# Performance work log

Hardware: AMD Instinct MI355X
Metric: run time of the kernel (lower is better)

Reference implementation:

```python
import jax, jax.numpy as jnp
import numpy as np

D = 1024        # d_hidden
DE = 512        # d_expert (routed)
E = 8           # n_routed_experts
TOP_K = 2
DS = DE * 2     # shared expert width = d_expert * n_shared_experts


def setup_inputs() -> dict:
    key = jax.random.key(0)
    ks = jax.random.split(key, 8)
    s = 1.0 / np.sqrt(D)
    return {
        "x": jax.random.normal(ks[0], (2, 1024, D), dtype=jnp.float32),
        "W_g": jax.random.normal(ks[1], (D, E), dtype=jnp.float32) * s,
        "Wg_e": jax.random.normal(ks[2], (E, D, DE), dtype=jnp.float32) * s,
        "Wu_e": jax.random.normal(ks[3], (E, D, DE), dtype=jnp.float32) * s,
        "Wd_e": jax.random.normal(ks[4], (E, DE, D), dtype=jnp.float32) * (1.0 / np.sqrt(DE)),
        "Wg_s": jax.random.normal(ks[5], (D, DS), dtype=jnp.float32) * s,
        "Wu_s": jax.random.normal(ks[6], (D, DS), dtype=jnp.float32) * s,
        "Wd_s": jax.random.normal(ks[7], (DS, D), dtype=jnp.float32) * (1.0 / np.sqrt(DS)),
    }


def _moe(x, W_g, Wg_e, Wu_e, Wd_e, Wg_s, Wu_s, Wd_s):
    B, T, Dm = x.shape
    N = B * T
    xf = x.reshape(N, Dm)

    # shared expert (SwiGLU)
    shared = (jax.nn.silu(xf @ Wg_s) * (xf @ Wu_s)) @ Wd_s  # [N, D]

    # gating: softmax then top-k (set membership identical to torch sorted=False)
    probs = jax.nn.softmax(xf @ W_g, axis=-1)               # [N, E]
    topk_vals, topk_ids = jax.lax.top_k(probs, TOP_K)       # [N, K]

    # combine weights c[n, e] = sum of topk_vals where routed to expert e
    # (equivalent to the original gather -> weighted scatter_add combine)
    c = jnp.zeros((N, E), dtype=x.dtype)
    c = c.at[jnp.arange(N)[:, None], topk_ids].add(topk_vals)

    # dense per-expert SwiGLU, weighted-combined (same math as gather/scatter loop)
    gate = jax.nn.silu(jnp.einsum('nd,edh->neh', xf, Wg_e))
    up = jnp.einsum('nd,edh->neh', xf, Wu_e)
    routed = jnp.einsum('neh,ne,ehd->nd', gate * up, c, Wd_e)  # [N, D]

    return (shared + routed).reshape(B, T, Dm)


def reference(x, W_g, Wg_e, Wu_e, Wd_e, Wg_s, Wu_s, Wd_s):
    return _moe(x, W_g, Wg_e, Wu_e, Wd_e, Wg_s, Wu_s, Wd_s)
```

## Files before the change

kernel.cpp:

```cpp
#include <hip/hip_runtime.h>
#include <hip/hip_bf16.h>

#define NTOK 2048
#define DIM  1024
#define DEXP 512
#define NEXP 8
#define DSH  1024
#define KH   5120
#define MAXROWS 5120
#define PACKBLOCKS 3840

typedef __hip_bfloat16 bf16;
typedef __attribute__((ext_vector_type(8))) short bf16x8;
typedef __attribute__((ext_vector_type(4))) float floatx4;

__device__ __forceinline__ void gl_lds16(const bf16* g, bf16* l) {
    __builtin_amdgcn_global_load_lds(
        (const __attribute__((address_space(1))) void*)g,
        (__attribute__((address_space(3))) void*)l, 16, 0, 0);
}

__device__ __forceinline__ float b2f(short s) {
    union { float f; unsigned u; } v;
    v.u = ((unsigned)(unsigned short)s) << 16;
    return v.f;
}

struct B4 { bf16 a, b, c, d; };

__global__ __launch_bounds__(128) void pack_gate(
        const float* __restrict__ Wg_s, const float* __restrict__ Wu_s,
        const float* __restrict__ Wg_e, const float* __restrict__ Wu_e,
        const float* __restrict__ Wd_s, const float* __restrict__ Wd_e,
        const float* __restrict__ x, const float* __restrict__ Wg,
        bf16* __restrict__ Bg, bf16* __restrict__ Bu, bf16* __restrict__ Bd,
        bf16* __restrict__ Xb, int2* __restrict__ te, float2* __restrict__ tp) {
    int b = blockIdx.x;
    const int tid = threadIdx.x;
    if (b < PACKBLOCKS) {
        __shared__ unsigned lt[64][35];
        const float* src; bf16* dst; int C; long dstStride, dstBase; int tilesX;
        if (b < 256)        { src = Wg_s; dst = Bg; C = 1024; dstStride = 1024; dstBase = 0; tilesX = 16; }
        else if (b < 1280)  { int z = (b - 256) >> 7; b = (b - 256) & 127;
                              src = Wg_e + (long)z * DIM * DEXP; dst = Bg; C = 512;
                              dstStride = 1024; dstBase = (long)(DSH + z * DEXP) * 1024; tilesX = 8; }
        else if (b < 1536)  { b -= 1280; src = Wu_s; dst = Bu; C = 1024; dstStride = 1024; dstBase = 0; tilesX = 16; }
        else if (b < 2560)  { int z = (b - 1536) >> 7; b = (b - 1536) & 127;
                              src = Wu_e + (long)z * DIM * DEXP; dst = Bu; C = 512;
                              dstStride = 1024; dstBase = (long)(DSH + z * DEXP) * 1024; tilesX = 8; }
        else if (b < 2816)  { b -= 2560; src = Wd_s; dst = Bd; C = 1024; dstStride = KH; dstBase = 0; tilesX = 16; }
        else                { int z = (b - 2816) >> 7; b = (b - 2816) & 127;
                              src = Wd_e + (long)z * DEXP * DIM; dst = Bd; C = 1024;
                              dstStride = KH; dstBase = DSH + (long)z * DEXP; tilesX = 16; }
        const int tileX = b & (tilesX - 1), tileY = b / tilesX;
        const int c0 = tileX * 64, r0 = tileY * 64;

        const int lrow = tid >> 4, lch = tid & 15;
#pragma unroll
        for (int i = 0; i < 8; i++) {
            int row = lrow + i * 8;
            float4 v = *(const float4*)(src + (long)(r0 + row) * C + c0 + lch * 4);
            union { bf16 h[2]; unsigned u; } p0, p1;
            p0.h[0] = __float2bfloat16(v.x); p0.h[1] = __float2bfloat16(v.y);
            p1.h[0] = __float2bfloat16(v.z); p1.h[1] = __float2bfloat16(v.w);
            lt[row][lch * 2]     = p0.u;
            lt[row][lch * 2 + 1] = p1.u;
        }
        __syncthreads();
        const int kc = tid & 7;
#pragma unroll
        for (int i = 0; i < 4; i++) {
            int h = (tid >> 3) + i * 16;
            union { unsigned short s[8]; bf16x8 v8; } o;
#pragma unroll
            for (int j = 0; j < 8; j++)
                o.s[j] = ((const unsigned short*)lt[kc * 8 + j])[h];
            *(bf16x8*)(dst + dstBase + (long)(c0 + h) * dstStride + r0 + kc * 8) = o.v8;
        }
    } else {
        int t = (b - PACKBLOCKS) * 2 + (tid >> 6);
        int lane = tid & 63;
        const float* xr = x + (long)t * DIM;
        bf16* xo = Xb + (long)t * DIM;
        float acc[NEXP] = {0.f, 0.f, 0.f, 0.f, 0.f, 0.f, 0.f, 0.f};
#pragma unroll
        for (int i = 0; i < 4; i++) {
            int d = lane * 4 + i * 256;
            float4 xv = *(const float4*)(xr + d);
            B4 o{__float2bfloat16(xv.x), __float2bfloat16(xv.y),
                 __float2bfloat16(xv.z), __float2bfloat16(xv.w)};
            *(B4*)(xo + d) = o;
#pragma unroll
            for (int j = 0; j < 4; j++) {
                float xs = (j == 0) ? xv.x : (j == 1) ? xv.y : (j == 2) ? xv.z : xv.w;
                float4 w0 = *(const float4*)(Wg + (d + j) * NEXP);
                float4 w1 = *(const float4*)(Wg + (d + j) * NEXP + 4);
                acc[0] += xs * w0.x; acc[1] += xs * w0.y; acc[2] += xs * w0.z; acc[3] += xs * w0.w;
                acc[4] += xs * w1.x; acc[5] += xs * w1.y; acc[6] += xs * w1.z; acc[7] += xs * w1.w;
            }
        }
#pragma unroll
        for (int e = 0; e < NEXP; e++)
#pragma unroll
            for (int off = 32; off; off >>= 1)
                acc[e] += __shfl_xor(acc[e], off);
        if (lane == 0) {
            float m = acc[0];
#pragma unroll
            for (int e = 1; e < NEXP; e++) m = fmaxf(m, acc[e]);
            float p[NEXP], s = 0.f;
#pragma unroll
            for (int e = 0; e < NEXP; e++) { p[e] = expf(acc[e] - m); s += p[e]; }
            float inv = 1.f / s;
#pragma unroll
            for (int e = 0; e < NEXP; e++) p[e] *= inv;
            int i1 = 0;
#pragma unroll
            for (int e = 1; e < NEXP; e++) if (p[e] > p[i1]) i1 = e;
            int i2 = (i1 == 0) ? 1 : 0;
#pragma unroll
            for (int e = 0; e < NEXP; e++) if (e != i1 && p[e] > p[i2]) i2 = e;
            te[t] = make_int2(i1, i2);
            tp[t] = make_float2(p[i1], p[i2]);
        }
    }
}

__global__ __launch_bounds__(512) void assign_kernel(const int2* __restrict__ te,
                                                     const float2* __restrict__ tp,
                                                     int* __restrict__ counts,
                                                     int* __restrict__ offs,
                                                     int* __restrict__ tok_list,
                                                     float* __restrict__ cw,
                                                     int* __restrict__ s1a,
                                                     int* __restrict__ s2a) {
    __shared__ int cnt[NEXP];
    const int e = threadIdx.x >> 6;
    const int lane = threadIdx.x & 63;
    int base = 0;
    for (int t0 = 0; t0 < NTOK; t0 += 64) {
        int t = t0 + lane;
        int2 ee = te[t];
        bool m1 = (ee.x == e), m2 = (ee.y == e);
        bool mt = m1 || m2;
        unsigned long long mask = __ballot(mt);
        int pre = __popcll(mask & ((1ull << lane) - 1ull));
        if (mt) {
            int slot = base + pre;
            tok_list[e * NTOK + slot] = t;
            float2 pp = tp[t];
            cw[e * NTOK + slot] = m1 ? pp.x : pp.y;
            if (m1) s1a[t] = slot; else s2a[t] = slot;
        }
        base += __popcll(mask);
    }
    if (lane == 0) cnt[e] = base;
    __syncthreads();
    if (threadIdx.x == 0) {
        int o = 0;
#pragma unroll
        for (int i = 0; i < NEXP; i++) {
            counts[i] = cnt[i];
            offs[i] = o;
            o += (cnt[i] + 127) & ~127;
        }
    }
}

__global__ __launch_bounds__(256) void gu_all(const bf16* __restrict__ X,
                                              const bf16* __restrict__ Bg,
                                              const bf16* __restrict__ Bu,
                                              const int* __restrict__ counts,
                                              const int* __restrict__ offs,
                                              const int* __restrict__ tok_list,
                                              const float* __restrict__ cw,
                                              bf16* __restrict__ Hs,
                                              bf16* __restrict__ He) {
    __shared__ __align__(16) bf16 sA[2][128 * 32];
    __shared__ __align__(16) bf16 sBg[2][64 * 32];
    __shared__ __align__(16) bf16 sBu[2][64 * 32];

    const int b = blockIdx.x;
    const bool routed = b < 1024;
    int e = 0, m, c;
    if (routed) {
        e = b >> 7; m = (b >> 3) & 15; c = b & 7;
        if (m * 128 >= counts[e]) return;
    } else {
        int bs = b - 1024; m = bs >> 4; c = bs & 15;
    }
    const int so = routed ? offs[e] : 0;
    const int colB0 = routed ? (DSH + e * DEXP + c * 64) : c * 64;

    const int tid = threadIdx.x;
    const int wave = tid >> 6, lane = tid & 63;
    const int wr = wave >> 1, wc = wave & 1;
    const int q = lane >> 4, l15 = lane & 15;
    const int koff = (q ^ ((l15 >> 1) & 3)) * 8;

    const int r0 = tid >> 2, c4 = tid & 3;
    const int r1 = r0 + 64;
    const int c4s = c4 ^ ((r0 >> 1) & 3);
    long aRow0, aRow1;
    if (routed) {
        const int* tl = tok_list + e * NTOK + m * 128;
        aRow0 = (long)tl[r0] * DIM;
        aRow1 = (long)tl[r1] * DIM;
    } else {
        aRow0 = (long)(m * 128 + r0) * DIM;
        aRow1 = (long)(m * 128 + r1) * DIM;
    }
    const long bRow = (long)(colB0 + r0) * DIM;

    floatx4 accG[4][2], accU[4][2];
    const floatx4 z4 = {0.f, 0.f, 0.f, 0.f};
#pragma unroll
    for (int i = 0; i < 4; i++)
#pragma unroll
        for (int j = 0; j < 2; j++) { accG[i][j] = z4; accU[i][j] = z4; }

    auto stage = [&](int bb, int k0) {
        gl_lds16(X + aRow0 + k0 + c4s * 8, &sA[bb][wave * 512]);
        gl_lds16(X + aRow1 + k0 + c4s * 8, &sA[bb][2048 + wave * 512]);
        gl_lds16(Bg + bRow + k0 + c4s * 8, &sBg[bb][wave * 512]);
        gl_lds16(Bu + bRow + k0 + c4s * 8, &sBu[bb][wave * 512]);
    };
    auto compute = [&](int bb) {
        bf16x8 af[4], bgv[2], buv[2];
#pragma unroll
        for (int rt = 0; rt < 4; rt++)
            af[rt] = *(const bf16x8*)(&sA[bb][(wr * 64 + rt * 16 + l15) * 32 + koff]);
#pragma unroll
        for (int ct = 0; ct < 2; ct++) {
            int cb = (wc * 32 + ct * 16 + l15) * 32 + koff;
            bgv[ct] = *(const bf16x8*)(&sBg[bb][cb]);
            buv[ct] = *(const bf16x8*)(&sBu[bb][cb]);
        }
#pragma unroll
        for (int rt = 0; rt < 4; rt++)
#pragma unroll
            for (int ct = 0; ct < 2; ct++) {
                accG[rt][ct] = __builtin_amdgcn_mfma_f32_16x16x32_bf16(af[rt], bgv[ct], accG[rt][ct], 0, 0, 0);
                accU[rt][ct] = __builtin_amdgcn_mfma_f32_16x16x32_bf16(af[rt], buv[ct], accU[rt][ct], 0, 0, 0);
            }
    };

    stage(0, 0);
    __syncthreads();
    int cur = 0;
    for (int ks = 0; ks < DIM / 32; ks++) {
        if (ks < DIM / 32 - 1) stage(cur ^ 1, (ks + 1) * 32);
        compute(cur);
        __syncthreads();
        cur ^= 1;
    }

    float wv[4][4];
#pragma unroll
    for (int rt = 0; rt < 4; rt++)
#pragma unroll
        for (int r = 0; r < 4; r++) {
            int srow = wr * 64 + rt * 16 + q * 4 + r;
            wv[rt][r] = routed ? cw[e * NTOK + m * 128 + srow] : 1.0f;
        }
#pragma unroll
    for (int rt = 0; rt < 4; rt++)
#pragma unroll
        for (int ct = 0; ct < 2; ct++)
#pragma unroll
            for (int r = 0; r < 4; r++) {
                int srow = wr * 64 + rt * 16 + q * 4 + r;
                int colLoc = c * 64 + wc * 32 + ct * 16 + l15;
                float g = accG[rt][ct][r];
                float u = accU[rt][ct][r];
                float h = (g / (1.f + __expf(-g))) * u * wv[rt][r];
                if (routed)
                    He[(long)(so + m * 128 + srow) * DEXP + colLoc] = __float2bfloat16(h);
                else
                    Hs[(long)(m * 128 + srow) * DSH + colLoc] = __float2bfloat16(h);
            }
}

__global__ __launch_bounds__(256) void down_all(const bf16* __restrict__ Hs,
                                                const bf16* __restrict__ He,
                                                const bf16* __restrict__ Bd,
                                                const int* __restrict__ counts,
                                                const int* __restrict__ offs,
                                                bf16* __restrict__ Ys,
                                                bf16* __restrict__ Ye) {
    __shared__ __align__(16) bf16 sA[2][128 * 32];
    __shared__ __align__(16) bf16 sB[2][64 * 32];

    const int b = blockIdx.x;
    const bool routed = b < 2048;
    int e = 0, m, cc;
    if (routed) {
        e = b >> 8; m = (b >> 4) & 15; cc = b & 15;
        if (m * 128 >= counts[e]) return;
    } else {
        int bs = b - 2048; m = bs >> 4; cc = bs & 15;
    }
    const int so = routed ? offs[e] : 0;
    const bf16* A = routed ? He + (long)so * DEXP : Hs;
    bf16* Y = routed ? Ye + (long)so * DIM : Ys;
    const int astr = routed ? DEXP : DSH;
    const int ksteps = routed ? (DEXP / 32) : (DSH / 32);
    const int kg0 = routed ? (DSH + e * DEXP) : 0;

    const int tid = threadIdx.x;
    const int wave = tid >> 6, lane = tid & 63;
    const int wr = wave >> 1, wc = wave & 1;
    const int q = lane >> 4, l15 = lane & 15;
    const int koff = (q ^ ((l15 >> 1) & 3)) * 8;

    const int r0 = tid >> 2, c4 = tid & 3;
    const int r1 = r0 + 64;
    const int c4s = c4 ^ ((r0 >> 1) & 3);
    const long aRow0 = (long)(m * 128 + r0) * astr;
    const long aRow1 = (long)(m * 128 + r1) * astr;
    const long bRow = (long)(cc * 64 + r0) * KH + kg0;

    floatx4 acc[4][2];
    const floatx4 z4 = {0.f, 0.f, 0.f, 0.f};
#pragma unroll
    for (int i = 0; i < 4; i++)
#pragma unroll
        for (int j = 0; j < 2; j++) acc[i][j] = z4;

    auto stage = [&](int bb, int k0) {
        gl_lds16(A + aRow0 + k0 + c4s * 8, &sA[bb][wave * 512]);
        gl_lds16(A + aRow1 + k0 + c4s * 8, &sA[bb][2048 + wave * 512]);
        gl_lds16(Bd + bRow + k0 + c4s * 8, &sB[bb][wave * 512]);
    };
    auto compute = [&](int bb) {
        bf16x8 af[4], bb2[2];
#pragma unroll
        for (int rt = 0; rt < 4; rt++)
            af[rt] = *(const bf16x8*)(&sA[bb][(wr * 64 + rt * 16 + l15) * 32 + koff]);
#pragma unroll
        for (int ct = 0; ct < 2; ct++)
            bb2[ct] = *(const bf16x8*)(&sB[bb][(wc * 32 + ct * 16 + l15) * 32 + koff]);
#pragma unroll
        for (int rt = 0; rt < 4; rt++)
#pragma unroll
            for (int ct = 0; ct < 2; ct++)
                acc[rt][ct] = __builtin_amdgcn_mfma_f32_16x16x32_bf16(af[rt], bb2[ct], acc[rt][ct], 0, 0, 0);
    };

    stage(0, 0);
    __syncthreads();
    int cur = 0;
    for (int ks = 0; ks < ksteps; ks++) {
        if (ks < ksteps - 1) stage(cur ^ 1, (ks + 1) * 32);
        compute(cur);
        __syncthreads();
        cur ^= 1;
    }

#pragma unroll
    for (int rt = 0; rt < 4; rt++)
#pragma unroll
        for (int ct = 0; ct < 2; ct++)
#pragma unroll
            for (int r = 0; r < 4; r++) {
                int srow = wr * 64 + rt * 16 + q * 4 + r;
                int mc = cc * 64 + wc * 32 + ct * 16 + l15;
                Y[(long)(m * 128 + srow) * DIM + mc] = __float2bfloat16(acc[rt][ct][r]);
            }
}

__global__ __launch_bounds__(256) void combine_kernel(const bf16* __restrict__ Ys,
                                                      const bf16* __restrict__ Ye,
                                                      const int2* __restrict__ te,
                                                      const int* __restrict__ s1a,
                                                      const int* __restrict__ s2a,
                                                      const int* __restrict__ offs,
                                                      float* __restrict__ out) {
    int idx = blockIdx.x * 256 + threadIdx.x;
    int t = idx >> 7;
    int d = (idx & 127) * 8;
    int2 ee = te[t];
    long r1 = (long)(offs[ee.x] + s1a[t]);
    long r2 = (long)(offs[ee.y] + s2a[t]);
    bf16x8 a = *(const bf16x8*)(Ys + (long)t * DIM + d);
    bf16x8 p = *(const bf16x8*)(Ye + r1 * DIM + d);
    bf16x8 r = *(const bf16x8*)(Ye + r2 * DIM + d);
    float* o = out + (long)t * DIM + d;
#pragma unroll
    for (int i = 0; i < 8; i++)
        o[i] = b2f(a[i]) + b2f(p[i]) + b2f(r[i]);
}

extern "C" void kernel_launch(void* const* d_in, const int* in_sizes, int n_in,
                              void* d_out, int out_size, void* d_ws, size_t ws_size,
                              hipStream_t stream) {
    const float* x    = (const float*)d_in[0];
    const float* W_g  = (const float*)d_in[1];
    const float* Wg_e = (const float*)d_in[2];
    const float* Wu_e = (const float*)d_in[3];
    const float* Wd_e = (const float*)d_in[4];
    const float* Wg_s = (const float*)d_in[5];
    const float* Wu_s = (const float*)d_in[6];
    const float* Wd_s = (const float*)d_in[7];
    float* out = (float*)d_out;

    bf16* Xb = (bf16*)d_ws;
    bf16* Bg = Xb + (size_t)NTOK * DIM;
    bf16* Bu = Bg + (size_t)KH * DIM;
    bf16* Bd = Bu + (size_t)KH * DIM;
    bf16* Hs = Bd + (size_t)DIM * KH;
    bf16* He = Hs + (size_t)NTOK * DSH;
    bf16* Ys = He + (size_t)MAXROWS * DEXP;
    bf16* Ye = Ys + (size_t)NTOK * DIM;
    int*  counts   = (int*)(Ye + (size_t)MAXROWS * DIM);
    int*  offs     = counts + NEXP;
    int*  tok_list = offs + NEXP;
    float* cw      = (float*)(tok_list + NEXP * NTOK);
    int*  s1a      = (int*)(cw + NEXP * NTOK);
    int*  s2a      = s1a + NTOK;
    int2* te       = (int2*)(s2a + NTOK);
    float2* tp     = (float2*)(te + NTOK);

    hipMemsetAsync(tok_list, 0,
                   sizeof(int) * NEXP * NTOK + sizeof(float) * NEXP * NTOK, stream);
    pack_gate<<<PACKBLOCKS + NTOK / 2, 128, 0, stream>>>(
        Wg_s, Wu_s, Wg_e, Wu_e, Wd_s, Wd_e, x, W_g, Bg, Bu, Bd, Xb, te, tp);
    assign_kernel<<<1, 512, 0, stream>>>(te, tp, counts, offs, tok_list, cw, s1a, s2a);
    gu_all<<<1280, 256, 0, stream>>>(Xb, Bg, Bu, counts, offs, tok_list, cw, Hs, He);
    down_all<<<2304, 256, 0, stream>>>(Hs, He, Bd, counts, offs, Ys, Ye);
    combine_kernel<<<NTOK * DIM / 8 / 256, 256, 0, stream>>>(Ys, Ye, te, s1a, s2a, offs, out);
}
```

Baseline: 213.3 us.

## Triple-buffer LDS staging with partial vmcnt waits in both GEMM kernels

Both the gate/up and down-projection GEMM kernels move from double to triple LDS buffering and prefetch two K-steps ahead. Each full __syncthreads is replaced by an explicit s_waitcnt vmcnt with a partial count plus raw barriers, so a thread waits only for the oldest stage's loads. The aim is to keep more global-to-LDS loads in flight and hide memory latency behind MFMA work. This costs about 50% more shared memory, which can lower occupancy, and the hand-written vmcnt counts must match the exact number of loads issued per stage.

```diff
diff --git a/kernel.cpp b/kernel.cpp
--- a/kernel.cpp
+++ b/kernel.cpp
@@ -176,9 +176,9 @@
                                               const float* __restrict__ cw,
                                               bf16* __restrict__ Hs,
                                               bf16* __restrict__ He) {
-    __shared__ __align__(16) bf16 sA[2][128 * 32];
-    __shared__ __align__(16) bf16 sBg[2][64 * 32];
-    __shared__ __align__(16) bf16 sBu[2][64 * 32];
+    __shared__ __align__(16) bf16 sA[3][128 * 32];
+    __shared__ __align__(16) bf16 sBg[3][64 * 32];
+    __shared__ __align__(16) bf16 sBu[3][64 * 32];
 
     const int b = blockIdx.x;
     const bool routed = b < 1024;
@@ -245,14 +245,21 @@
             }
     };
 
+    const int NS = DIM / 32;
     stage(0, 0);
-    __syncthreads();
-    int cur = 0;
-    for (int ks = 0; ks < DIM / 32; ks++) {
-        if (ks < DIM / 32 - 1) stage(cur ^ 1, (ks + 1) * 32);
-        compute(cur);
-        __syncthreads();
-        cur ^= 1;
+    stage(1, 32);
+    int bb = 0;
+    for (int ks = 0; ks < NS; ks++) {
+        if (ks + 2 < NS) stage((bb + 2) % 3, (ks + 2) * 32);
+        if (ks + 2 < NS)      asm volatile("s_waitcnt vmcnt(8)" ::: "memory");
+        else if (ks + 1 < NS) asm volatile("s_waitcnt vmcnt(4)" ::: "memory");
+        else                  asm volatile("s_waitcnt vmcnt(0)" ::: "memory");
+        __builtin_amdgcn_s_barrier();
+        asm volatile("" ::: "memory");
+        compute(bb);
+        asm volatile("" ::: "memory");
+        __builtin_amdgcn_s_barrier();
+        bb = (bb + 1) % 3;
     }
 
     float wv[4][4];
@@ -288,8 +295,8 @@
                                                 const int* __restrict__ offs,
                                                 bf16* __restrict__ Ys,
                                                 bf16* __restrict__ Ye) {
-    __shared__ __align__(16) bf16 sA[2][128 * 32];
-    __shared__ __align__(16) bf16 sB[2][64 * 32];
+    __shared__ __align__(16) bf16 sA[3][128 * 32];
+    __shared__ __align__(16) bf16 sB[3][64 * 32];
 
     const int b = blockIdx.x;
     const bool routed = b < 2048;
@@ -348,13 +355,19 @@
     };
 
     stage(0, 0);
-    __syncthreads();
-    int cur = 0;
+    stage(1, 32);
+    int bb = 0;
     for (int ks = 0; ks < ksteps; ks++) {
-        if (ks < ksteps - 1) stage(cur ^ 1, (ks + 1) * 32);
-        compute(cur);
-        __syncthreads();
-        cur ^= 1;
+        if (ks + 2 < ksteps) stage((bb + 2) % 3, (ks + 2) * 32);
+        if (ks + 2 < ksteps)      asm volatile("s_waitcnt vmcnt(6)" ::: "memory");
+        else if (ks + 1 < ksteps) asm volatile("s_waitcnt vmcnt(3)" ::: "memory");
+        else                      asm volatile("s_waitcnt vmcnt(0)" ::: "memory");
+        __builtin_amdgcn_s_barrier();
+        asm volatile("" ::: "memory");
+        compute(bb);
+        asm volatile("" ::: "memory");
+        __builtin_amdgcn_s_barrier();
+        bb = (bb + 1) % 3;
     }
 
 #pragma unroll
```

New measurement: 209.7 us. Within noise of the previous version (-1.7%).

## Double K-tile depth to 64, use partial vmcnt waits, drop memset

Applied to the files above, without the earlier changes.

Both GEMM kernels (gate/up and down) now stage 64-wide K tiles instead of 32 and use a row-XOR swizzle for the LDS layout. The prefetch loop waits with explicit s_waitcnt vmcnt counts so the next tile's loads can stay in flight while the current tile computes, which halves the number of barriers per K. The hipMemsetAsync of tok_list/cw is removed; assign_kernel now zero-fills only the padding up to each expert's 128-row boundary. This doubles LDS use per block, which may lower occupancy.

```diff
diff --git a/kernel.cpp b/kernel.cpp
--- a/kernel.cpp
+++ b/kernel.cpp
@@ -154,6 +154,11 @@
         }
         base += __popcll(mask);
     }
+    int rounded = (base + 127) & ~127;
+    for (int s = base + lane; s < rounded; s += 64) {
+        tok_list[e * NTOK + s] = 0;
+        cw[e * NTOK + s] = 0.f;
+    }
     if (lane == 0) cnt[e] = base;
     __syncthreads();
     if (threadIdx.x == 0) {
@@ -176,9 +181,9 @@
                                               const float* __restrict__ cw,
                                               bf16* __restrict__ Hs,
                                               bf16* __restrict__ He) {
-    __shared__ __align__(16) bf16 sA[2][128 * 32];
-    __shared__ __align__(16) bf16 sBg[2][64 * 32];
-    __shared__ __align__(16) bf16 sBu[2][64 * 32];
+    __shared__ __align__(16) bf16 sA[2][128 * 64];
+    __shared__ __align__(16) bf16 sBg[2][64 * 64];
+    __shared__ __align__(16) bf16 sBu[2][64 * 64];
 
     const int b = blockIdx.x;
     const bool routed = b < 1024;
@@ -196,21 +201,21 @@
     const int wave = tid >> 6, lane = tid & 63;
     const int wr = wave >> 1, wc = wave & 1;
     const int q = lane >> 4, l15 = lane & 15;
-    const int koff = (q ^ ((l15 >> 1) & 3)) * 8;
-
-    const int r0 = tid >> 2, c4 = tid & 3;
-    const int r1 = r0 + 64;
-    const int c4s = c4 ^ ((r0 >> 1) & 3);
-    long aRow0, aRow1;
-    if (routed) {
-        const int* tl = tok_list + e * NTOK + m * 128;
-        aRow0 = (long)tl[r0] * DIM;
-        aRow1 = (long)tl[r1] * DIM;
-    } else {
-        aRow0 = (long)(m * 128 + r0) * DIM;
-        aRow1 = (long)(m * 128 + r1) * DIM;
-    }
-    const long bRow = (long)(colB0 + r0) * DIM;
+
+    const int strow = tid >> 3, sc = tid & 7;
+    long aOff[4], bOff[2];
+#pragma unroll
+    for (int s = 0; s < 4; s++) {
+        int row = s * 32 + strow;
+        long r = routed ? (long)tok_list[e * NTOK + m * 128 + row]
+                        : (long)(m * 128 + row);
+        aOff[s] = r * DIM + (sc ^ (row & 7)) * 8;
+    }
+#pragma unroll
+    for (int s = 0; s < 2; s++) {
+        int row = s * 32 + strow;
+        bOff[s] = (long)(colB0 + row) * DIM + (sc ^ (row & 7)) * 8;
+    }
 
     floatx4 accG[4][2], accU[4][2];
     const floatx4 z4 = {0.f, 0.f, 0.f, 0.f};
@@ -220,38 +225,56 @@
         for (int j = 0; j < 2; j++) { accG[i][j] = z4; accU[i][j] = z4; }
 
     auto stage = [&](int bb, int k0) {
-        gl_lds16(X + aRow0 + k0 + c4s * 8, &sA[bb][wave * 512]);
-        gl_lds16(X + aRow1 + k0 + c4s * 8, &sA[bb][2048 + wave * 512]);
-        gl_lds16(Bg + bRow + k0 + c4s * 8, &sBg[bb][wave * 512]);
-        gl_lds16(Bu + bRow + k0 + c4s * 8, &sBu[bb][wave * 512]);
+#pragma unroll
+        for (int s = 0; s < 4; s++)
+            gl_lds16(X + aOff[s] + k0, &sA[bb][s * 2048 + wave * 512]);
+#pragma unroll
+        for (int s = 0; s < 2; s++) {
+            gl_lds16(Bg + bOff[s] + k0, &sBg[bb][s * 2048 + wave * 512]);
+            gl_lds16(Bu + bOff[s] + k0, &sBu[bb][s * 2048 + wave * 512]);
+        }
     };
     auto compute = [&](int bb) {
-        bf16x8 af[4], bgv[2], buv[2];
-#pragma unroll
-        for (int rt = 0; rt < 4; rt++)
-            af[rt] = *(const bf16x8*)(&sA[bb][(wr * 64 + rt * 16 + l15) * 32 + koff]);
-#pragma unroll
-        for (int ct = 0; ct < 2; ct++) {
-            int cb = (wc * 32 + ct * 16 + l15) * 32 + koff;
-            bgv[ct] = *(const bf16x8*)(&sBg[bb][cb]);
-            buv[ct] = *(const bf16x8*)(&sBu[bb][cb]);
-        }
-#pragma unroll
-        for (int rt = 0; rt < 4; rt++)
+#pragma unroll
+        for (int kk = 0; kk < 2; kk++) {
+            bf16x8 af[4], bgv[2], buv[2];
+#pragma unroll
+            for (int rt = 0; rt < 4; rt++) {
+                int row = wr * 64 + rt * 16 + l15;
+                af[rt] = *(const bf16x8*)(&sA[bb][row * 64 + (((kk * 4 + q) ^ (row & 7)) * 8)]);
+            }
 #pragma unroll
             for (int ct = 0; ct < 2; ct++) {
-                accG[rt][ct] = __builtin_amdgcn_mfma_f32_16x16x32_bf16(af[rt], bgv[ct], accG[rt][ct], 0, 0, 0);
-                accU[rt][ct] = __builtin_amdgcn_mfma_f32_16x16x32_bf16(af[rt], buv[ct], accU[rt][ct], 0, 0, 0);
-            }
+                int row = wc * 32 + ct * 16 + l15;
+                int off = row * 64 + (((kk * 4 + q) ^ (row & 7)) * 8);
+                bgv[ct] = *(const bf16x8*)(&sBg[bb][off]);
+                buv[ct] = *(const bf16x8*)(&sBu[bb][off]);
+            }
+#pragma unroll
+            for (int rt = 0; rt < 4; rt++)
+#pragma unroll
+                for (int ct = 0; ct < 2; ct++) {
+                    accG[rt][ct] = __builtin_amdgcn_mfma_f32_16x16x32_bf16(af[rt], bgv[ct], accG[rt][ct], 0, 0, 0);
+                    accU[rt][ct] = __builtin_amdgcn_mfma_f32_16x16x32_bf16(af[rt], buv[ct], accU[rt][ct], 0, 0, 0);
+                }
+        }
     };
 
+    const int NS = DIM / 64;
     stage(0, 0);
-    __syncthreads();
     int cur = 0;
-    for (int ks = 0; ks < DIM / 32; ks++) {
-        if (ks < DIM / 32 - 1) stage(cur ^ 1, (ks + 1) * 32);
+    for (int ks = 0; ks < NS; ks++) {
+        if (ks + 1 < NS) {
+            stage(cur ^ 1, (ks + 1) * 64);
+            asm volatile("s_waitcnt vmcnt(8)" ::: "memory");
+        } else {
+            asm volatile("s_waitcnt vmcnt(0)" ::: "memory");
+        }
+        __builtin_amdgcn_s_barrier();
+        asm volatile("" ::: "memory");
         compute(cur);
-        __syncthreads();
+        asm volatile("" ::: "memory");
+        __builtin_amdgcn_s_barrier();
         cur ^= 1;
     }
 
@@ -288,8 +311,8 @@
                                                 const int* __restrict__ offs,
                                                 bf16* __restrict__ Ys,
                                                 bf16* __restrict__ Ye) {
-    __shared__ __align__(16) bf16 sA[2][128 * 32];
-    __shared__ __align__(16) bf16 sB[2][64 * 32];
+    __shared__ __align__(16) bf16 sA[2][128 * 64];
+    __shared__ __align__(16) bf16 sB[2][64 * 64];
 
     const int b = blockIdx.x;
     const bool routed = b < 2048;
@@ -304,21 +327,26 @@
     const bf16* A = routed ? He + (long)so * DEXP : Hs;
     bf16* Y = routed ? Ye + (long)so * DIM : Ys;
     const int astr = routed ? DEXP : DSH;
-    const int ksteps = routed ? (DEXP / 32) : (DSH / 32);
+    const int ksteps = routed ? (DEXP / 64) : (DSH / 64);
     const int kg0 = routed ? (DSH + e * DEXP) : 0;
 
     const int tid = threadIdx.x;
     const int wave = tid >> 6, lane = tid & 63;
     const int wr = wave >> 1, wc = wave & 1;
     const int q = lane >> 4, l15 = lane & 15;
-    const int koff = (q ^ ((l15 >> 1) & 3)) * 8;
-
-    const int r0 = tid >> 2, c4 = tid & 3;
-    const int r1 = r0 + 64;
-    const int c4s = c4 ^ ((r0 >> 1) & 3);
-    const long aRow0 = (long)(m * 128 + r0) * astr;
-    const long aRow1 = (long)(m * 128 + r1) * astr;
-    const long bRow = (long)(cc * 64 + r0) * KH + kg0;
+
+    const int strow = tid >> 3, sc = tid & 7;
+    long aOff[4], bOff[2];
+#pragma unroll
+    for (int s = 0; s < 4; s++) {
+        int row = s * 32 + strow;
+        aOff[s] = (long)(m * 128 + row) * astr + (sc ^ (row & 7)) * 8;
+    }
+#pragma unroll
+    for (int s = 0; s < 2; s++) {
+        int row = s * 32 + strow;
+        bOff[s] = (long)(cc * 64 + row) * KH + kg0 + (sc ^ (row & 7)) * 8;
+    }
 
     floatx4 acc[4][2];
     const floatx4 z4 = {0.f, 0.f, 0.f, 0.f};
@@ -328,32 +356,49 @@
         for (int j = 0; j < 2; j++) acc[i][j] = z4;
 
     auto stage = [&](int bb, int k0) {
-        gl_lds16(A + aRow0 + k0 + c4s * 8, &sA[bb][wave * 512]);
-        gl_lds16(A + aRow1 + k0 + c4s * 8, &sA[bb][2048 + wave * 512]);
-        gl_lds16(Bd + bRow + k0 + c4s * 8, &sB[bb][wave * 512]);
+#pragma unroll
+        for (int s = 0; s < 4; s++)
+            gl_lds16(A + aOff[s] + k0, &sA[bb][s * 2048 + wave * 512]);
+#pragma unroll
+        for (int s = 0; s < 2; s++)
+            gl_lds16(Bd + bOff[s] + k0, &sB[bb][s * 2048 + wave * 512]);
     };
     auto compute = [&](int bb) {
-        bf16x8 af[4], bb2[2];
-#pragma unroll
-        for (int rt = 0; rt < 4; rt++)
-            af[rt] = *(const bf16x8*)(&sA[bb][(wr * 64 + rt * 16 + l15) * 32 + koff]);
-#pragma unroll
-        for (int ct = 0; ct < 2; ct++)
-            bb2[ct] = *(const bf16x8*)(&sB[bb][(wc * 32 + ct * 16 + l15) * 32 + koff]);
-#pragma unroll
-        for (int rt = 0; rt < 4; rt++)
-#pragma unroll
-            for (int ct = 0; ct < 2; ct++)
-                acc[rt][ct] = __builtin_amdgcn_mfma_f32_16x16x32_bf16(af[rt], bb2[ct], acc[rt][ct], 0, 0, 0);
+#pragma unroll
+        for (int kk = 0; kk < 2; kk++) {
+            bf16x8 af[4], bb2[2];
+#pragma unroll
+            for (int rt = 0; rt < 4; rt++) {
+                int row = wr * 64 + rt * 16 + l15;
+                af[rt] = *(const bf16x8*)(&sA[bb][row * 64 + (((kk * 4 + q) ^ (row & 7)) * 8)]);
+            }
+#pragma unroll
+            for (int ct = 0; ct < 2; ct++) {
+                int row = wc * 32 + ct * 16 + l15;
+                bb2[ct] = *(const bf16x8*)(&sB[bb][row * 64 + (((kk * 4 + q) ^ (row & 7)) * 8)]);
+            }
+#pragma unroll
+            for (int rt = 0; rt < 4; rt++)
+#pragma unroll
+                for (int ct = 0; ct < 2; ct++)
+                    acc[rt][ct] = __builtin_amdgcn_mfma_f32_16x16x32_bf16(af[rt], bb2[ct], acc[rt][ct], 0, 0, 0);
+        }
     };
 
     stage(0, 0);
-    __syncthreads();
     int cur = 0;
     for (int ks = 0; ks < ksteps; ks++) {
-        if (ks < ksteps - 1) stage(cur ^ 1, (ks + 1) * 32);
+        if (ks + 1 < ksteps) {
+            stage(cur ^ 1, (ks + 1) * 64);
+            asm volatile("s_waitcnt vmcnt(6)" ::: "memory");
+        } else {
+            asm volatile("s_waitcnt vmcnt(0)" ::: "memory");
+        }
+        __builtin_amdgcn_s_barrier();
+        asm volatile("" ::: "memory");
         compute(cur);
-        __syncthreads();
+        asm volatile("" ::: "memory");
+        __builtin_amdgcn_s_barrier();
         cur ^= 1;
     }
 
@@ -421,8 +466,6 @@
     int2* te       = (int2*)(s2a + NTOK);
     float2* tp     = (float2*)(te + NTOK);
 
-    hipMemsetAsync(tok_list, 0,
-                   sizeof(int) * NEXP * NTOK + sizeof(float) * NEXP * NTOK, stream);
     pack_gate<<<PACKBLOCKS + NTOK / 2, 128, 0, stream>>>(
         Wg_s, Wu_s, Wg_e, Wu_e, Wd_s, Wd_e, x, W_g, Bg, Bu, Bd, Xb, te, tp);
     assign_kernel<<<1, 512, 0, stream>>>(te, tp, counts, offs, tok_list, cw, s1a, s2a);
```

Measured after the change: 216.0 us. No clear change (+1.2%).
